# Kernel optimization log

Hardware: AMD Instinct MI355X
Metric: run time of the kernel (lower is better)

Reference implementation:

```python
import jax, jax.numpy as jnp
import numpy as np

B, T, E = 64, 64, 512
D_MODEL = 2 * E          # 1024, mamba d_model (concat of spatial+temporal)
D_INNER = 2 * D_MODEL    # 2048
D_STATE = 16
DT_RANK = D_MODEL // 16  # 64
K_CONV = 4


def setup_inputs() -> dict:
    key = jax.random.key(0)
    ks = jax.random.split(key, 12)
    def n(k, shape, scale=0.02):
        return jax.random.normal(k, shape, jnp.float32) * scale
    return {
        "spatial_features": jax.random.normal(ks[0], (B, T, E), jnp.float32),
        "temporal_features": jax.random.normal(ks[1], (B, T, E), jnp.float32),
        "W_in": n(ks[2], (D_MODEL, 2 * D_INNER)),
        "conv_w": n(ks[3], (D_INNER, K_CONV)),
        "conv_b": jnp.zeros((D_INNER,), jnp.float32),
        "W_x": n(ks[4], (D_INNER, DT_RANK + 2 * D_STATE)),
        "W_dt": n(ks[5], (DT_RANK, D_INNER)),
        "b_dt": jnp.zeros((D_INNER,), jnp.float32),
        "A_log": n(ks[6], (D_INNER, D_STATE)),   # A = -exp(A_log) ~ -1
        "D_skip": jnp.ones((D_INNER,), jnp.float32),
        "W_out": n(ks[7], (D_INNER, D_MODEL)),
        "W1": n(ks[8], (D_MODEL, 512)),
        "b1": jnp.zeros((512,), jnp.float32),
        "W2": n(ks[9], (512, 256)),
        "b2": jnp.zeros((256,), jnp.float32),
        "W3": n(ks[10], (256, 6)),
        "b3": jnp.zeros((6,), jnp.float32),
    }


def _mamba(x, W_in, conv_w, conv_b, W_x, W_dt, b_dt, A_log, D_skip, W_out):
    # x: (B, T, d_model) -> (B, T, d_model). Standard Mamba selective-scan block.
    Bsz = x.shape[0]
    xz = jnp.einsum('btd,de->bte', x, W_in)            # (B,T,2*d_inner)
    xi, z = jnp.split(xz, 2, axis=-1)
    # causal depthwise conv1d over T
    xt = jnp.pad(jnp.swapaxes(xi, 1, 2), ((0, 0), (0, 0), (K_CONV - 1, 0)))
    conv = jax.lax.conv_general_dilated(
        xt, conv_w[:, None, :], (1,), 'VALID', feature_group_count=D_INNER)
    xc = jax.nn.silu(jnp.swapaxes(conv, 1, 2) + conv_b)  # (B,T,d_inner)
    proj = jnp.einsum('btd,de->bte', xc, W_x)            # (B,T,dt_rank+2n)
    dt_raw, Bs, Cs = jnp.split(proj, [DT_RANK, DT_RANK + D_STATE], axis=-1)
    dt = jax.nn.softplus(jnp.einsum('btr,rd->btd', dt_raw, W_dt) + b_dt)
    A = -jnp.exp(A_log)                                  # (d_inner, n)

    def step(h, inputs):
        dt_t, B_t, C_t, x_t = inputs                     # (B,d),(B,n),(B,n),(B,d)
        dA = jnp.exp(dt_t[..., None] * A)                # (B,d,n)
        h = dA * h + (dt_t * x_t)[..., None] * B_t[:, None, :]
        y = jnp.einsum('bdn,bn->bd', h, C_t)
        return h, y

    xs = (jnp.swapaxes(dt, 0, 1), jnp.swapaxes(Bs, 0, 1),
          jnp.swapaxes(Cs, 0, 1), jnp.swapaxes(xc, 0, 1))
    h0 = jnp.zeros((Bsz, D_INNER, D_STATE), xc.dtype)
    _, ys = jax.lax.scan(step, h0, xs)
    y = jnp.swapaxes(ys, 0, 1) + xc * D_skip
    y = y * jax.nn.silu(z)
    return jnp.einsum('btd,de->bte', y, W_out)


def reference(spatial_features, temporal_features, W_in, conv_w, conv_b, W_x,
              W_dt, b_dt, A_log, D_skip, W_out, W1, b1, W2, b2, W3, b3):
    # concat -> final Mamba -> per-frame MLP head (vectorized over B,T)
    x = jnp.concatenate([spatial_features, temporal_features], axis=-1)  # (B,T,2E)
    f = _mamba(x, W_in, conv_w, conv_b, W_x, W_dt, b_dt, A_log, D_skip, W_out)
    h1 = jax.nn.relu(f @ W1 + b1)
    h2 = jax.nn.relu(h1 @ W2 + b2)
    return h2 @ W3 + b3  # (B,T,6)
```

## Files before the change

### kernel.cpp

```cpp
#include <hip/hip_runtime.h>
#include <hip/hip_bf16.h>
#include <math.h>

#define B_   64
#define T_   64
#define E_   512
#define DM   1024
#define DI   2048
#define DS   16
#define DTR  64
#define M_   4096

typedef __hip_bfloat16 bf16;
typedef __attribute__((ext_vector_type(8))) short bf16x8;
typedef __attribute__((ext_vector_type(4))) float f32x4;

template<int SPLITK, int BM, int BN>
__global__ __launch_bounds__(256) void gemm_mfma(
    const bf16* __restrict__ A, int lda,
    const bf16* __restrict__ Bt, int ldb,
    float* __restrict__ Cv, int ldc,
    int Ndim, int Kdim)
{
    __shared__ __align__(16) bf16 As[BM * 32];
    __shared__ __align__(16) bf16 Bs[BN * 32];
    const int tid  = threadIdx.x;
    const int wave = tid >> 6;
    const int lane = tid & 63;
    const int bm = blockIdx.y * BM;
    const int bn = blockIdx.x * BN;
    const int lrow = lane >> 2;
    const int lkc  = (lane & 3) * 8;
    constexpr int RPW = (BM + BN) / 4;
    constexpr int NI  = RPW / 16;
    constexpr int WMT = BM / 32;
    constexpr int WNT = BN / 32;
    const int wm = (wave >> 1) * (BM / 2);
    const int wn = (wave & 1) * (BN / 2);
    const int fm = lane & 15;
    const int fq = lane >> 4;

    int kstart = 0, kend = Kdim;
    if (SPLITK > 1) {
        int chunk = Kdim / SPLITK;
        kstart = blockIdx.z * chunk;
        kend = kstart + chunk;
    }

    f32x4 acc[WMT][WNT];
    #pragma unroll
    for (int i = 0; i < WMT; ++i)
        #pragma unroll
        for (int j = 0; j < WNT; ++j)
            acc[i][j] = (f32x4){0.f, 0.f, 0.f, 0.f};

    for (int k0 = kstart; k0 < kend; k0 += 32) {
        #pragma unroll
        for (int i = 0; i < NI; ++i) {
            int rowbase = wave * RPW + i * 16;
            int row = rowbase + lrow;
            if (rowbase < BM) {
                const bf16* ga = A + (size_t)(bm + row) * lda + k0 + lkc;
                __builtin_amdgcn_global_load_lds(
                    (const __attribute__((address_space(1))) void*)ga,
                    (__attribute__((address_space(3))) void*)&As[rowbase * 32],
                    16, 0, 0);
            } else {
                int brow = bn + row - BM;
                if (brow >= Ndim) brow = Ndim - 1;
                const bf16* gb = Bt + (size_t)brow * ldb + k0 + lkc;
                __builtin_amdgcn_global_load_lds(
                    (const __attribute__((address_space(1))) void*)gb,
                    (__attribute__((address_space(3))) void*)&Bs[(rowbase - BM) * 32],
                    16, 0, 0);
            }
        }
        __syncthreads();
        bf16x8 a[WMT], b[WNT];
        #pragma unroll
        for (int i = 0; i < WMT; ++i)
            a[i] = *(const bf16x8*)&As[(wm + i * 16 + fm) * 32 + fq * 8];
        #pragma unroll
        for (int j = 0; j < WNT; ++j)
            b[j] = *(const bf16x8*)&Bs[(wn + j * 16 + fm) * 32 + fq * 8];
        #pragma unroll
        for (int i = 0; i < WMT; ++i)
            #pragma unroll
            for (int j = 0; j < WNT; ++j)
                acc[i][j] = __builtin_amdgcn_mfma_f32_16x16x32_bf16(
                    a[i], b[j], acc[i][j], 0, 0, 0);
        __syncthreads();
    }

    size_t zoff = (SPLITK > 1) ? (size_t)blockIdx.z * M_ * ldc : 0;
    #pragma unroll
    for (int i = 0; i < WMT; ++i) {
        int rowb = bm + wm + i * 16 + fq * 4;
        #pragma unroll
        for (int j = 0; j < WNT; ++j) {
            int col = bn + wn + j * 16 + fm;
            if (col < Ndim) {
                #pragma unroll
                for (int r = 0; r < 4; ++r)
                    Cv[zoff + (size_t)(rowb + r) * ldc + col] = acc[i][j][r];
            }
        }
    }
}

__global__ __launch_bounds__(256) void gemm_g1_conv(
    const bf16* __restrict__ A,
    const bf16* __restrict__ Bt,
    bf16* __restrict__ xcb,
    bf16* __restrict__ zb,
    const float* __restrict__ conv_w,
    const float* __restrict__ conv_b,
    const bf16* __restrict__ W1T,
    const bf16* __restrict__ Wob,
    bf16* __restrict__ WcT,
    const bf16* __restrict__ WxT,
    float* __restrict__ proj)
{
    constexpr int XS = 136;
    __shared__ __align__(16) bf16 smem[128 * XS];
    const int tid  = threadIdx.x;
    const int wave = tid >> 6;
    const int lane = tid & 63;
    const int lrow = lane >> 2;
    const int lkc  = (lane & 3) * 8;
    const int wm = (wave >> 1) * 64;
    const int fm = lane & 15;
    const int fq = lane >> 4;

    if (blockIdx.x >= 32) {
        const int fbm = (blockIdx.x - 32) * 128;
        const int fbn = blockIdx.y * 64;
        const int fwn = (wave & 1) * 32;
        f32x4 facc[4][2];
        #pragma unroll
        for (int i = 0; i < 4; ++i)
            #pragma unroll
            for (int j = 0; j < 2; ++j)
                facc[i][j] = (f32x4){0.f, 0.f, 0.f, 0.f};

        for (int k0 = 0; k0 < 1024; k0 += 32) {
            #pragma unroll
            for (int i = 0; i < 3; ++i) {
                int rowbase = wave * 48 + i * 16;
                int row = rowbase + lrow;
                if (rowbase < 128) {
                    const bf16* ga = W1T + (size_t)(fbm + row) * 1024 + k0 + lkc;
                    __builtin_amdgcn_global_load_lds(
                        (const __attribute__((address_space(1))) void*)ga,
                        (__attribute__((address_space(3))) void*)&smem[rowbase * 32],
                        16, 0, 0);
                } else {
                    const bf16* gb = Wob + (size_t)(fbn + row - 128) * 1024 + k0 + lkc;
                    __builtin_amdgcn_global_load_lds(
                        (const __attribute__((address_space(1))) void*)gb,
                        (__attribute__((address_space(3))) void*)&smem[4096 + (rowbase - 128) * 32],
                        16, 0, 0);
                }
            }
            __syncthreads();
            bf16x8 a[4], b[2];
            #pragma unroll
            for (int i = 0; i < 4; ++i)
                a[i] = *(const bf16x8*)&smem[(wm + i * 16 + fm) * 32 + fq * 8];
            #pragma unroll
            for (int j = 0; j < 2; ++j)
                b[j] = *(const bf16x8*)&smem[4096 + (fwn + j * 16 + fm) * 32 + fq * 8];
            #pragma unroll
            for (int i = 0; i < 4; ++i)
                #pragma unroll
                for (int j = 0; j < 2; ++j)
                    facc[i][j] = __builtin_amdgcn_mfma_f32_16x16x32_bf16(
                        a[i], b[j], facc[i][j], 0, 0, 0);
            __syncthreads();
        }
        #pragma unroll
        for (int i = 0; i < 4; ++i) {
            int rowb = fbm + wm + i * 16 + fq * 4;
            #pragma unroll
            for (int j = 0; j < 2; ++j) {
                int col = fbn + fwn + j * 16 + fm;
                #pragma unroll
                for (int r = 0; r < 4; ++r)
                    WcT[(size_t)(rowb + r) * 2048 + col] =
                        __float2bfloat16(facc[i][j][r]);
            }
        }
        return;
    }

    const int bm = blockIdx.y * 128;
    const int bn = blockIdx.x * 128;
    const int wn = (wave & 1) * 64;

    f32x4 acc[4][4];
    #pragma unroll
    for (int i = 0; i < 4; ++i)
        #pragma unroll
        for (int j = 0; j < 4; ++j)
            acc[i][j] = (f32x4){0.f, 0.f, 0.f, 0.f};

    for (int k0 = 0; k0 < 1024; k0 += 32) {
        #pragma unroll
        for (int i = 0; i < 4; ++i) {
            int rowbase = wave * 64 + i * 16;
            int row = rowbase + lrow;
            if (rowbase < 128) {
                const bf16* ga = A + (size_t)(bm + row) * 1024 + k0 + lkc;
                __builtin_amdgcn_global_load_lds(
                    (const __attribute__((address_space(1))) void*)ga,
                    (__attribute__((address_space(3))) void*)&smem[rowbase * 32],
                    16, 0, 0);
            } else {
                const bf16* gb = Bt + (size_t)(bn + row - 128) * 1024 + k0 + lkc;
                __builtin_amdgcn_global_load_lds(
                    (const __attribute__((address_space(1))) void*)gb,
                    (__attribute__((address_space(3))) void*)&smem[4096 + (rowbase - 128) * 32],
                    16, 0, 0);
            }
        }
        __syncthreads();
        bf16x8 a[4], b[4];
        #pragma unroll
        for (int i = 0; i < 4; ++i)
            a[i] = *(const bf16x8*)&smem[(wm + i * 16 + fm) * 32 + fq * 8];
        #pragma unroll
        for (int j = 0; j < 4; ++j)
            b[j] = *(const bf16x8*)&smem[4096 + (wn + j * 16 + fm) * 32 + fq * 8];
        #pragma unroll
        for (int i = 0; i < 4; ++i)
            #pragma unroll
            for (int j = 0; j < 4; ++j)
                acc[i][j] = __builtin_amdgcn_mfma_f32_16x16x32_bf16(
                    a[i], b[j], acc[i][j], 0, 0, 0);
        __syncthreads();
    }

    if (bn < 2048) {
        #pragma unroll
        for (int i = 0; i < 4; ++i) {
            int rowb = wm + i * 16 + fq * 4;
            #pragma unroll
            for (int j = 0; j < 4; ++j) {
                int col = wn + j * 16 + fm;
                #pragma unroll
                for (int r = 0; r < 4; ++r)
                    smem[(rowb + r) * XS + col] = __float2bfloat16(acc[i][j][r]);
            }
        }
        __syncthreads();
        {
            int col = tid & 127;
            int seq = tid >> 7;
            int gcol = bn + col;
            float4 cw = *(const float4*)&conv_w[gcol * 4];
            float cb = conv_b[gcol];
            float w0 = 0.f, w1 = 0.f, w2 = 0.f;
            int base = seq * 64;
            for (int t = 0; t < 64; ++t) {
                int idx = (base + t) * XS + col;
                float cur = __bfloat162float(smem[idx]);
                float cacc = cb;
                cacc = fmaf(w0, cw.x, cacc); cacc = fmaf(w1, cw.y, cacc);
                cacc = fmaf(w2, cw.z, cacc); cacc = fmaf(cur, cw.w, cacc);
                smem[idx] = __float2bfloat16(__fdividef(cacc, 1.f + __expf(-cacc)));
                w0 = w1; w1 = w2; w2 = cur;
            }
        }
        __syncthreads();
        #pragma unroll
        for (int it = 0; it < 8; ++it) {
            int g = it * 256 + tid;
            int row = g >> 4;
            int cg = (g & 15) * 8;
            bf16x8 v = *(const bf16x8*)&smem[row * XS + cg];
            *(bf16x8*)&xcb[(size_t)(bm + row) * 2048 + bn + cg] = v;
        }
        {
            const int mw = wave * 32;
            f32x4 dacc[2][6];
            #pragma unroll
            for (int i = 0; i < 2; ++i)
                #pragma unroll
                for (int j = 0; j < 6; ++j)
                    dacc[i][j] = (f32x4){0.f, 0.f, 0.f, 0.f};
            #pragma unroll
            for (int kit = 0; kit < 4; ++kit) {
                bf16x8 bfrag[6], afrag[2];
                #pragma unroll
                for (int j = 0; j < 6; ++j)
                    bfrag[j] = *(const bf16x8*)(WxT
                        + (size_t)(j * 16 + fm) * 2048 + bn + kit * 32 + fq * 8);
                #pragma unroll
                for (int i = 0; i < 2; ++i)
                    afrag[i] = *(const bf16x8*)&smem[
                        (mw + i * 16 + fm) * XS + kit * 32 + fq * 8];
                #pragma unroll
                for (int i = 0; i < 2; ++i)
                    #pragma unroll
                    for (int j = 0; j < 6; ++j)
                        dacc[i][j] = __builtin_amdgcn_mfma_f32_16x16x32_bf16(
                            afrag[i], bfrag[j], dacc[i][j], 0, 0, 0);
            }
            #pragma unroll
            for (int i = 0; i < 2; ++i) {
                int rowb = bm + mw + i * 16 + fq * 4;
                #pragma unroll
                for (int j = 0; j < 6; ++j) {
                    int n = j * 16 + fm;
                    #pragma unroll
                    for (int r = 0; r < 4; ++r)
                        atomicAdd(&proj[(size_t)(rowb + r) * 96 + n],
                                  dacc[i][j][r]);
                }
            }
        }
    } else {
        #pragma unroll
        for (int i = 0; i < 4; ++i) {
            int rowb = bm + wm + i * 16 + fq * 4;
            #pragma unroll
            for (int j = 0; j < 4; ++j) {
                int col = bn - 2048 + wn + j * 16 + fm;
                #pragma unroll
                for (int r = 0; r < 4; ++r)
                    zb[(size_t)(rowb + r) * 2048 + col] =
                        __float2bfloat16(acc[i][j][r]);
            }
        }
    }
}

__global__ __launch_bounds__(256) void scan_g3_kernel(
    const float* __restrict__ proj,
    const bf16*  __restrict__ WdT,
    const float* __restrict__ b_dt,
    bf16* __restrict__ xcy,
    const bf16*  __restrict__ zb,
    const float* __restrict__ A_log,
    const float* __restrict__ D_skip)
{
    __shared__ float BC[64][32];
    __shared__ __align__(16) bf16 Adt[64 * 64];
    __shared__ __align__(16) bf16 Bdt[256 * 64];
    const int tid  = threadIdx.x;
    const int wave = tid >> 6;
    const int lane = tid & 63;
    const int b  = blockIdx.y;
    const int dg = blockIdx.x;
    const int fm = lane & 15;
    const int fq = lane >> 4;

    for (int i = tid; i < 64 * 32; i += 256) {
        int t = i >> 5, c = i & 31;
        BC[t][c] = proj[(size_t)(b * 64 + t) * 96 + 64 + c];
    }
    {
        int arow = tid >> 2;
        int ak = (tid & 3) * 16;
        const float* ga = proj + (size_t)(b * 64 + arow) * 96 + ak;
        float4 v0 = *(const float4*)(ga + 0);
        float4 v1 = *(const float4*)(ga + 4);
        float4 v2 = *(const float4*)(ga + 8);
        float4 v3 = *(const float4*)(ga + 12);
        bf16 o[16] = {
            __float2bfloat16(v0.x), __float2bfloat16(v0.y),
            __float2bfloat16(v0.z), __float2bfloat16(v0.w),
            __float2bfloat16(v1.x), __float2bfloat16(v1.y),
            __float2bfloat16(v1.z), __float2bfloat16(v1.w),
            __float2bfloat16(v2.x), __float2bfloat16(v2.y),
            __float2bfloat16(v2.z), __float2bfloat16(v2.w),
            __float2bfloat16(v3.x), __float2bfloat16(v3.y),
            __float2bfloat16(v3.z), __float2bfloat16(v3.w)};
        *(bf16x8*)&Adt[arow * 64 + ak]     = *(const bf16x8*)&o[0];
        *(bf16x8*)&Adt[arow * 64 + ak + 8] = *(const bf16x8*)&o[8];
    }
    #pragma unroll
    for (int i = 0; i < 8; ++i) {
        int rowbase = wave * 64 + i * 8;
        const bf16* gb = WdT + (size_t)(dg * 256 + rowbase + (lane >> 3)) * 64
                             + (lane & 7) * 8;
        __builtin_amdgcn_global_load_lds(
            (const __attribute__((address_space(1))) void*)gb,
            (__attribute__((address_space(3))) void*)&Bdt[rowbase * 64],
            16, 0, 0);
    }
    __syncthreads();

    f32x4 acc[4][4];
    #pragma unroll
    for (int i = 0; i < 4; ++i)
        #pragma unroll
        for (int j = 0; j < 4; ++j)
            acc[i][j] = (f32x4){0.f, 0.f, 0.f, 0.f};
    #pragma unroll
    for (int k0 = 0; k0 < 64; k0 += 32) {
        bf16x8 a[4], bfr[4];
        #pragma unroll
        for (int i = 0; i < 4; ++i)
            a[i] = *(const bf16x8*)&Adt[(i * 16 + fm) * 64 + k0 + fq * 8];
        #pragma unroll
        for (int j = 0; j < 4; ++j)
            bfr[j] = *(const bf16x8*)&Bdt[(wave * 64 + j * 16 + fm) * 64 + k0 + fq * 8];
        #pragma unroll
        for (int i = 0; i < 4; ++i)
            #pragma unroll
            for (int j = 0; j < 4; ++j)
                acc[i][j] = __builtin_amdgcn_mfma_f32_16x16x32_bf16(
                    a[i], bfr[j], acc[i][j], 0, 0, 0);
    }
    __syncthreads();
    bf16* dt_s = Bdt;
    #pragma unroll
    for (int j = 0; j < 4; ++j) {
        int dloc = wave * 64 + j * 16 + fm;
        float bv = b_dt[dg * 256 + dloc];
        #pragma unroll
        for (int i = 0; i < 4; ++i) {
            #pragma unroll
            for (int r = 0; r < 4; ++r) {
                int t = i * 16 + fq * 4 + r;
                float v = acc[i][j][r] + bv;
                v = (v > 20.f) ? v : __logf(1.f + __expf(v));
                dt_s[t * 256 + dloc] = __float2bfloat16(v);
            }
        }
    }
    __syncthreads();

    const int d = dg * 256 + tid;
    float av[16];
    const float4* alp = (const float4*)(A_log + d * 16);
    *(float4*)&av[0]  = alp[0];
    *(float4*)&av[4]  = alp[1];
    *(float4*)&av[8]  = alp[2];
    *(float4*)&av[12] = alp[3];
    float A[16];
    #pragma unroll
    for (int n = 0; n < 16; ++n) A[n] = -__expf(av[n]);
    const float Dv = D_skip[d];
    float h[16];
    #pragma unroll
    for (int n = 0; n < 16; ++n) h[n] = 0.f;

    #pragma unroll 2
    for (int t = 0; t < T_; ++t) {
        int row = b * T_ + t;
        size_t off = (size_t)row * DI + d;
        float xv = __bfloat162float(xcy[off]);
        float dt = __bfloat162float(dt_s[t * 256 + tid]);
        float dtx = dt * xv;
        float y = 0.f;
        #pragma unroll
        for (int n = 0; n < 16; ++n) {
            float dA = __expf(dt * A[n]);
            h[n] = fmaf(dA, h[n], dtx * BC[t][n]);
            y = fmaf(h[n], BC[t][16 + n], y);
        }
        float sk = fmaf(xv, Dv, y);
        float z = __bfloat162float(zb[off]);
        float g = __fdividef(z, 1.f + __expf(-z));
        xcy[off] = __float2bfloat16(sk * g);
    }
}

__global__ __launch_bounds__(256) void gemm_g6(
    const float* __restrict__ p5,
    const bf16* __restrict__ W2T,
    float* __restrict__ p6,
    const float* __restrict__ b1)
{
    __shared__ __align__(16) bf16 As[128 * 32];
    __shared__ __align__(16) bf16 Bs[128 * 32];
    const int tid  = threadIdx.x;
    const int wave = tid >> 6;
    const int lane = tid & 63;
    const int bm = blockIdx.y * 128;
    const int bn = blockIdx.x * 128;
    const int lrow = lane >> 2;
    const int lkc  = (lane & 3) * 8;
    const int wm = (wave >> 1) * 64;
    const int wn = (wave & 1) * 64;
    const int fm = lane & 15;
    const int fq = lane >> 4;
    const int kstart = blockIdx.z * 128;

    f32x4 acc[4][4];
    #pragma unroll
    for (int i = 0; i < 4; ++i)
        #pragma unroll
        for (int j = 0; j < 4; ++j)
            acc[i][j] = (f32x4){0.f, 0.f, 0.f, 0.f};

    for (int k0 = kstart; k0 < kstart + 128; k0 += 32) {
        #pragma unroll
        for (int i = 0; i < 2; ++i) {
            int rowbase = wave * 32 + i * 16;
            const bf16* gb = W2T + (size_t)(bn + rowbase + lrow) * 512 + k0 + lkc;
            __builtin_amdgcn_global_load_lds(
                (const __attribute__((address_space(1))) void*)gb,
                (__attribute__((address_space(3))) void*)&Bs[rowbase * 32],
                16, 0, 0);
        }
        #pragma unroll
        for (int p = 0; p < 4; ++p) {
            int idx = p * 256 + tid;
            int arow = idx >> 3;
            int ak4 = (idx & 7) * 4;
            const float* ga = p5 + (size_t)(bm + arow) * 512 + k0 + ak4;
            float4 u0 = *(const float4*)ga;
            float4 u1 = *(const float4*)(ga + 2097152);
            float4 u2 = *(const float4*)(ga + 4194304);
            float4 u3 = *(const float4*)(ga + 6291456);
            float4 bb = *(const float4*)(b1 + k0 + ak4);
            bf16 o[4] = {
                __float2bfloat16(fmaxf(u0.x + u1.x + u2.x + u3.x + bb.x, 0.f)),
                __float2bfloat16(fmaxf(u0.y + u1.y + u2.y + u3.y + bb.y, 0.f)),
                __float2bfloat16(fmaxf(u0.z + u1.z + u2.z + u3.z + bb.z, 0.f)),
                __float2bfloat16(fmaxf(u0.w + u1.w + u2.w + u3.w + bb.w, 0.f))};
            *(short4*)&As[arow * 32 + ak4] = *(const short4*)o;
        }
        __syncthreads();
        bf16x8 a[4], b[4];
        #pragma unroll
        for (int i = 0; i < 4; ++i)
            a[i] = *(const bf16x8*)&As[(wm + i * 16 + fm) * 32 + fq * 8];
        #pragma unroll
        for (int j = 0; j < 4; ++j)
            b[j] = *(const bf16x8*)&Bs[(wn + j * 16 + fm) * 32 + fq * 8];
        #pragma unroll
        for (int i = 0; i < 4; ++i)
            #pragma unroll
            for (int j = 0; j < 4; ++j)
                acc[i][j] = __builtin_amdgcn_mfma_f32_16x16x32_bf16(
                    a[i], b[j], acc[i][j], 0, 0, 0);
        __syncthreads();
    }

    size_t zoff = (size_t)blockIdx.z * M_ * 256;
    #pragma unroll
    for (int i = 0; i < 4; ++i) {
        int rowb = bm + wm + i * 16 + fq * 4;
        #pragma unroll
        for (int j = 0; j < 4; ++j) {
            int col = bn + wn + j * 16 + fm;
            #pragma unroll
            for (int r = 0; r < 4; ++r)
                p6[zoff + (size_t)(rowb + r) * 256 + col] = acc[i][j][r];
        }
    }
}

__global__ __launch_bounds__(256) void prep_kernel(
    const float* __restrict__ sp, const float* __restrict__ tp,
    bf16* __restrict__ xb, float* __restrict__ proj,
    const float* __restrict__ W_in,  bf16* __restrict__ WinT,
    const float* __restrict__ W_out, bf16* __restrict__ Wob,
    const float* __restrict__ W_x,   bf16* __restrict__ WxT,
    const float* __restrict__ W_dt,  bf16* __restrict__ WdT,
    const float* __restrict__ W1,    bf16* __restrict__ W1T,
    const float* __restrict__ W2,    bf16* __restrict__ W2T)
{
    __shared__ float tile[32][33];
    const int b = blockIdx.x;
    const int tid = threadIdx.x;
    if (b < 4096) {
        int idx = b * 256 + tid;
        int row = idx >> 8;
        int c4 = (idx & 255) * 4;
        const float* src = (c4 < 512) ? (sp + (size_t)row * 512 + c4)
                                      : (tp + (size_t)row * 512 + (c4 - 512));
        float4 v = *(const float4*)src;
        bf16* dst = xb + (size_t)row * 1024 + c4;
        dst[0] = __float2bfloat16(v.x); dst[1] = __float2bfloat16(v.y);
        dst[2] = __float2bfloat16(v.z); dst[3] = __float2bfloat16(v.w);
        if (idx < 98304)
            *(float4*)(proj + (size_t)idx * 4) = make_float4(0.f, 0.f, 0.f, 0.f);
        return;
    }
    if (b < 6144) {
        int idx = (b - 4096) * 1024 + tid * 4;
        float4 v = *(const float4*)(W_out + idx);
        bf16 o[4] = {__float2bfloat16(v.x), __float2bfloat16(v.y),
                     __float2bfloat16(v.z), __float2bfloat16(v.w)};
        *(short4*)&Wob[idx] = *(short4*)o;
        return;
    }
    const float* W; bf16* Wt; int K, N, tb;
    if      (b < 6336) { W = W_x;  Wt = WxT;  K = 2048; N = 96;   tb = b - 6144; }
    else if (b < 6464) { W = W_dt; Wt = WdT;  K = 64;   N = 2048; tb = b - 6336; }
    else if (b < 6976) { W = W1;   Wt = W1T;  K = 1024; N = 512;  tb = b - 6464; }
    else if (b < 7104) { W = W2;   Wt = W2T;  K = 512;  N = 256;  tb = b - 6976; }
    else               { W = W_in; Wt = WinT; K = 1024; N = 4096; tb = b - 7104; }
    int nb = N / 32;
    int bn = (tb % nb) * 32, bk = (tb / nb) * 32;
    int tx = tid & 31, ty = tid >> 5;
    #pragma unroll
    for (int i = 0; i < 32; i += 8)
        tile[ty + i][tx] = W[(size_t)(bk + ty + i) * N + bn + tx];
    __syncthreads();
    #pragma unroll
    for (int i = 0; i < 32; i += 8)
        Wt[(size_t)(bn + ty + i) * K + bk + tx] = __float2bfloat16(tile[tx][ty + i]);
}

template<int P>
__global__ __launch_bounds__(256) void head_kernel(
    const float* __restrict__ p6, int stride,
    const float* __restrict__ b2,
    const float* __restrict__ W3, const float* __restrict__ b3,
    float* __restrict__ out)
{
    int row = blockIdx.x * 4 + (threadIdx.x >> 6);
    int lane = threadIdx.x & 63;
    float acc[6] = {0.f, 0.f, 0.f, 0.f, 0.f, 0.f};
    #pragma unroll
    for (int kk = 0; kk < 4; ++kk) {
        int c = lane + kk * 64;
        size_t off = (size_t)row * 256 + c;
        float s = p6[off];
        #pragma unroll
        for (int p = 1; p < P; ++p) s += p6[(size_t)p * stride + off];
        s = fmaxf(s + b2[c], 0.f);
        #pragma unroll
        for (int n = 0; n < 6; ++n) acc[n] = fmaf(s, W3[c * 6 + n], acc[n]);
    }
    #pragma unroll
    for (int n = 0; n < 6; ++n) {
        float v = acc[n];
        #pragma unroll
        for (int off = 32; off > 0; off >>= 1) v += __shfl_down(v, off);
        if (lane == 0) out[(size_t)row * 6 + n] = v + b3[n];
    }
}

extern "C" void kernel_launch(void* const* d_in, const int* in_sizes, int n_in,
                              void* d_out, int out_size, void* d_ws, size_t ws_size,
                              hipStream_t stream)
{
    const float* spatial  = (const float*)d_in[0];
    const float* temporal = (const float*)d_in[1];
    const float* W_in     = (const float*)d_in[2];
    const float* conv_w   = (const float*)d_in[3];
    const float* conv_b   = (const float*)d_in[4];
    const float* W_x      = (const float*)d_in[5];
    const float* W_dt     = (const float*)d_in[6];
    const float* b_dt     = (const float*)d_in[7];
    const float* A_log    = (const float*)d_in[8];
    const float* D_skip   = (const float*)d_in[9];
    const float* W_out    = (const float*)d_in[10];
    const float* W1       = (const float*)d_in[11];
    const float* b1       = (const float*)d_in[12];
    const float* W2       = (const float*)d_in[13];
    const float* b2       = (const float*)d_in[14];
    const float* W3       = (const float*)d_in[15];
    const float* b3       = (const float*)d_in[16];
    float* out = (float*)d_out;

    char* w = (char*)d_ws;
    bf16*  xcb  = (bf16*)(w);
    bf16*  zb   = (bf16*)(w + 16777216);
    float* p5   = (float*)(w + 33554432);
    bf16*  xb   = (bf16*)(w + 67108864);
    bf16*  WinT = (bf16*)(w + 75497472);
    float* p6   = (float*)(w + 67108864);
    bf16*  WcT  = (bf16*)(w + 83886080);
    bf16*  W1T  = (bf16*)(w + 85983232);
    bf16*  W2T  = (bf16*)(w + 87031808);
    bf16*  WxT  = (bf16*)(w + 87293952);
    bf16*  WdT  = (bf16*)(w + 87687168);
    float* proj = (float*)(w + 87949312);
    bf16*  Wob  = (bf16*)(w + 89522176);

    dim3 blk(256);

    prep_kernel<<<dim3(11200), blk, 0, stream>>>(
        spatial, temporal, xb, proj, W_in, WinT, W_out, Wob,
        W_x, WxT, W_dt, WdT, W1, W1T, W2, W2T);

    gemm_g1_conv<<<dim3(36, 32), blk, 0, stream>>>(
        xb, WinT, xcb, zb, conv_w, conv_b, W1T, Wob, WcT, WxT, proj);

    scan_g3_kernel<<<dim3(8, 64), blk, 0, stream>>>(
        proj, WdT, b_dt, xcb, zb, A_log, D_skip);

    gemm_mfma<4, 128, 128><<<dim3(4, 32, 4), blk, 0, stream>>>(
        xcb, 2048, WcT, 2048, p5, 512, 512, 2048);

    gemm_g6<<<dim3(2, 32, 4), blk, 0, stream>>>(p5, W2T, p6, b1);

    head_kernel<4><<<dim3(1024), blk, 0, stream>>>(
        p6, 1048576, b2, W3, b3, out);
}
```

Before: 274.4 us.

## Drop split-K in head GEMMs, fuse bias+ReLU epilogue with bf16 outputs

The two MLP-head GEMMs no longer use split-K with fp32 partial buffers that the next kernel reduces. They now run full-K with 128x64 tiles, add bias and apply ReLU in the epilogue, and write bf16 activations directly. The head kernel then reads bf16 h2 instead of summing four fp32 partials. This removes a large amount of fp32 partial-sum traffic, in exchange for fewer blocks (256 and 128) with longer K loops, which lowers parallelism on the GPU.

```diff
diff --git a/kernel.cpp b/kernel.cpp
--- a/kernel.cpp
+++ b/kernel.cpp
@@ -15,11 +15,16 @@
 typedef __attribute__((ext_vector_type(8))) short bf16x8;
 typedef __attribute__((ext_vector_type(4))) float f32x4;
 
-template<int SPLITK, int BM, int BN>
+__device__ __forceinline__ float b2f(unsigned short s) {
+    return __uint_as_float(((unsigned)s) << 16);
+}
+
+template<int BM, int BN, int ACT, int OUTBF>
 __global__ __launch_bounds__(256) void gemm_mfma(
     const bf16* __restrict__ A, int lda,
     const bf16* __restrict__ Bt, int ldb,
-    float* __restrict__ Cv, int ldc,
+    void* __restrict__ Cv, int ldc,
+    const float* __restrict__ bias,
     int Ndim, int Kdim)
 {
     __shared__ __align__(16) bf16 As[BM * 32];
@@ -40,13 +45,6 @@
     const int fm = lane & 15;
     const int fq = lane >> 4;
 
-    int kstart = 0, kend = Kdim;
-    if (SPLITK > 1) {
-        int chunk = Kdim / SPLITK;
-        kstart = blockIdx.z * chunk;
-        kend = kstart + chunk;
-    }
-
     f32x4 acc[WMT][WNT];
     #pragma unroll
     for (int i = 0; i < WMT; ++i)
@@ -54,7 +52,7 @@
         for (int j = 0; j < WNT; ++j)
             acc[i][j] = (f32x4){0.f, 0.f, 0.f, 0.f};
 
-    for (int k0 = kstart; k0 < kend; k0 += 32) {
+    for (int k0 = 0; k0 < Kdim; k0 += 32) {
         #pragma unroll
         for (int i = 0; i < NI; ++i) {
             int rowbase = wave * RPW + i * 16;
@@ -92,7 +90,6 @@
         __syncthreads();
     }
 
-    size_t zoff = (SPLITK > 1) ? (size_t)blockIdx.z * M_ * ldc : 0;
     #pragma unroll
     for (int i = 0; i < WMT; ++i) {
         int rowb = bm + wm + i * 16 + fq * 4;
@@ -100,9 +97,15 @@
         for (int j = 0; j < WNT; ++j) {
             int col = bn + wn + j * 16 + fm;
             if (col < Ndim) {
-                #pragma unroll
-                for (int r = 0; r < 4; ++r)
-                    Cv[zoff + (size_t)(rowb + r) * ldc + col] = acc[i][j][r];
+                float bv = bias ? bias[col] : 0.f;
+                #pragma unroll
+                for (int r = 0; r < 4; ++r) {
+                    float v = acc[i][j][r] + bv;
+                    if (ACT == 1) v = fmaxf(v, 0.f);
+                    size_t off = (size_t)(rowb + r) * ldc + col;
+                    if (OUTBF) ((bf16*)Cv)[off] = __float2bfloat16(v);
+                    else       ((float*)Cv)[off] = v;
+                }
             }
         }
     }
@@ -465,93 +468,6 @@
         float z = __bfloat162float(zb[off]);
         float g = __fdividef(z, 1.f + __expf(-z));
         xcy[off] = __float2bfloat16(sk * g);
-    }
-}
-
-__global__ __launch_bounds__(256) void gemm_g6(
-    const float* __restrict__ p5,
-    const bf16* __restrict__ W2T,
-    float* __restrict__ p6,
-    const float* __restrict__ b1)
-{
-    __shared__ __align__(16) bf16 As[128 * 32];
-    __shared__ __align__(16) bf16 Bs[128 * 32];
-    const int tid  = threadIdx.x;
-    const int wave = tid >> 6;
-    const int lane = tid & 63;
-    const int bm = blockIdx.y * 128;
-    const int bn = blockIdx.x * 128;
-    const int lrow = lane >> 2;
-    const int lkc  = (lane & 3) * 8;
-    const int wm = (wave >> 1) * 64;
-    const int wn = (wave & 1) * 64;
-    const int fm = lane & 15;
-    const int fq = lane >> 4;
-    const int kstart = blockIdx.z * 128;
-
-    f32x4 acc[4][4];
-    #pragma unroll
-    for (int i = 0; i < 4; ++i)
-        #pragma unroll
-        for (int j = 0; j < 4; ++j)
-            acc[i][j] = (f32x4){0.f, 0.f, 0.f, 0.f};
-
-    for (int k0 = kstart; k0 < kstart + 128; k0 += 32) {
-        #pragma unroll
-        for (int i = 0; i < 2; ++i) {
-            int rowbase = wave * 32 + i * 16;
-            const bf16* gb = W2T + (size_t)(bn + rowbase + lrow) * 512 + k0 + lkc;
-            __builtin_amdgcn_global_load_lds(
-                (const __attribute__((address_space(1))) void*)gb,
-                (__attribute__((address_space(3))) void*)&Bs[rowbase * 32],
-                16, 0, 0);
-        }
-        #pragma unroll
-        for (int p = 0; p < 4; ++p) {
-            int idx = p * 256 + tid;
-            int arow = idx >> 3;
-            int ak4 = (idx & 7) * 4;
-            const float* ga = p5 + (size_t)(bm + arow) * 512 + k0 + ak4;
-            float4 u0 = *(const float4*)ga;
-            float4 u1 = *(const float4*)(ga + 2097152);
-            float4 u2 = *(const float4*)(ga + 4194304);
-            float4 u3 = *(const float4*)(ga + 6291456);
-            float4 bb = *(const float4*)(b1 + k0 + ak4);
-            bf16 o[4] = {
-                __float2bfloat16(fmaxf(u0.x + u1.x + u2.x + u3.x + bb.x, 0.f)),
-                __float2bfloat16(fmaxf(u0.y + u1.y + u2.y + u3.y + bb.y, 0.f)),
-                __float2bfloat16(fmaxf(u0.z + u1.z + u2.z + u3.z + bb.z, 0.f)),
-                __float2bfloat16(fmaxf(u0.w + u1.w + u2.w + u3.w + bb.w, 0.f))};
-            *(short4*)&As[arow * 32 + ak4] = *(const short4*)o;
-        }
-        __syncthreads();
-        bf16x8 a[4], b[4];
-        #pragma unroll
-        for (int i = 0; i < 4; ++i)
-            a[i] = *(const bf16x8*)&As[(wm + i * 16 + fm) * 32 + fq * 8];
-        #pragma unroll
-        for (int j = 0; j < 4; ++j)
-            b[j] = *(const bf16x8*)&Bs[(wn + j * 16 + fm) * 32 + fq * 8];
-        #pragma unroll
-        for (int i = 0; i < 4; ++i)
-            #pragma unroll
-            for (int j = 0; j < 4; ++j)
-                acc[i][j] = __builtin_amdgcn_mfma_f32_16x16x32_bf16(
-                    a[i], b[j], acc[i][j], 0, 0, 0);
-        __syncthreads();
-    }
-
-    size_t zoff = (size_t)blockIdx.z * M_ * 256;
-    #pragma unroll
-    for (int i = 0; i < 4; ++i) {
-        int rowb = bm + wm + i * 16 + fq * 4;
-        #pragma unroll
-        for (int j = 0; j < 4; ++j) {
-            int col = bn + wn + j * 16 + fm;
-            #pragma unroll
-            for (int r = 0; r < 4; ++r)
-                p6[zoff + (size_t)(rowb + r) * 256 + col] = acc[i][j][r];
-        }
     }
 }
 
@@ -608,24 +524,18 @@
         Wt[(size_t)(bn + ty + i) * K + bk + tx] = __float2bfloat16(tile[tx][ty + i]);
 }
 
-template<int P>
 __global__ __launch_bounds__(256) void head_kernel(
-    const float* __restrict__ p6, int stride,
-    const float* __restrict__ b2,
-    const float* __restrict__ W3, const float* __restrict__ b3,
-    float* __restrict__ out)
+    const bf16* __restrict__ h2, const float* __restrict__ W3,
+    const float* __restrict__ b3, float* __restrict__ out)
 {
     int row = blockIdx.x * 4 + (threadIdx.x >> 6);
     int lane = threadIdx.x & 63;
+    const bf16* hr = h2 + (size_t)row * 256;
     float acc[6] = {0.f, 0.f, 0.f, 0.f, 0.f, 0.f};
     #pragma unroll
     for (int kk = 0; kk < 4; ++kk) {
         int c = lane + kk * 64;
-        size_t off = (size_t)row * 256 + c;
-        float s = p6[off];
-        #pragma unroll
-        for (int p = 1; p < P; ++p) s += p6[(size_t)p * stride + off];
-        s = fmaxf(s + b2[c], 0.f);
+        float s = __bfloat162float(hr[c]);
         #pragma unroll
         for (int n = 0; n < 6; ++n) acc[n] = fmaf(s, W3[c * 6 + n], acc[n]);
     }
@@ -664,10 +574,10 @@
     char* w = (char*)d_ws;
     bf16*  xcb  = (bf16*)(w);
     bf16*  zb   = (bf16*)(w + 16777216);
-    float* p5   = (float*)(w + 33554432);
+    bf16*  h1   = (bf16*)(w + 33554432);
+    bf16*  h2   = (bf16*)(w + 37748736);
     bf16*  xb   = (bf16*)(w + 67108864);
     bf16*  WinT = (bf16*)(w + 75497472);
-    float* p6   = (float*)(w + 67108864);
     bf16*  WcT  = (bf16*)(w + 83886080);
     bf16*  W1T  = (bf16*)(w + 85983232);
     bf16*  W2T  = (bf16*)(w + 87031808);
@@ -688,11 +598,11 @@
     scan_g3_kernel<<<dim3(8, 64), blk, 0, stream>>>(
         proj, WdT, b_dt, xcb, zb, A_log, D_skip);
 
-    gemm_mfma<4, 128, 128><<<dim3(4, 32, 4), blk, 0, stream>>>(
-        xcb, 2048, WcT, 2048, p5, 512, 512, 2048);
-
-    gemm_g6<<<dim3(2, 32, 4), blk, 0, stream>>>(p5, W2T, p6, b1);
-
-    head_kernel<4><<<dim3(1024), blk, 0, stream>>>(
-        p6, 1048576, b2, W3, b3, out);
+    gemm_mfma<128, 64, 1, 1><<<dim3(8, 32), blk, 0, stream>>>(
+        xcb, 2048, WcT, 2048, h1, 512, b1, 512, 2048);
+
+    gemm_mfma<128, 64, 1, 1><<<dim3(4, 32), blk, 0, stream>>>(
+        h1, 512, W2T, 512, h2, 256, b2, 256, 512);
+
+    head_kernel<<<dim3(1024), blk, 0, stream>>>(h2, W3, b3, out);
 }
```

Result: slower. 282.4 us (+2.9%).
